# Optimization experiments

Measured on AMD Instinct MI355X. Metric: run time of the kernel, lower is better.

Reference implementation:

```python
import jax, jax.numpy as jnp
import numpy as np

EPS = 1e-5

def layer_norm(x, g, b):
    m = jnp.mean(x, axis=-1, keepdims=True)
    v = jnp.var(x, axis=-1, keepdims=True)
    return (x - m) / jnp.sqrt(v + EPS) * g + b

def mab(Q, K, adj, Wq, Wk, Wv, Wo, g1, b1, g2, b2, H):
    # Q: [B, nq, dq], K: [B, nk, dk], adj: [nk, nk] graph-conv aggregation
    B, nq, _ = Q.shape
    dv = Wq.shape[1]
    dh = dv // H
    Qp = Q @ Wq                                   # [B, nq, dv]
    Kg = jnp.einsum('ij,bjd->bid', adj, K)        # GCN neighborhood aggregation
    Kp = Kg @ Wk                                  # [B, nk, dv]
    Vp = Kg @ Wv                                  # [B, nk, dv]
    Qh = Qp.reshape(B, nq, H, dh)
    Kh = Kp.reshape(B, -1, H, dh)
    Vh = Vp.reshape(B, -1, H, dh)
    scale = 1.0 / np.sqrt(dv).astype(np.float32)
    att = jax.nn.softmax(jnp.einsum('bqhd,bkhd->bhqk', Qh, Kh) * scale, axis=-1)
    Oh = Qh + jnp.einsum('bhqk,bkhd->bqhd', att, Vh)   # residual inside heads
    O = Oh.reshape(B, nq, dv)
    O = layer_norm(O, g1, b1)
    O = O + jax.nn.relu(O @ Wo)
    O = layer_norm(O, g2, b2)
    return O

def setup_inputs() -> dict:
    key = jax.random.key(0)
    ks = jax.random.split(key, 16)
    B, P, D = 16384, 25, 256
    w = lambda k, shp: jax.random.normal(k, shp, dtype=jnp.float32) * 0.05
    adj2 = jax.random.uniform(ks[15], (3, 3), dtype=jnp.float32)
    adj2 = adj2 / jnp.sum(adj2, axis=-1, keepdims=True)  # row-normalized GCN adj
    return {
        'X': jax.random.normal(ks[0], (B, 1, D), dtype=jnp.float32),
        'S1': w(ks[1], (3, 1)),
        'S2': w(ks[2], (P, 3)),
        'adj1': jnp.ones((1, 1), dtype=jnp.float32),
        'adj2': adj2,
        'Wq1': w(ks[3], (D, D)), 'Wk1': w(ks[4], (D, D)),
        'Wv1': w(ks[5], (D, D)), 'Wo1': w(ks[6], (D, D)),
        'g11': jnp.ones((D,), jnp.float32), 'b11': jnp.zeros((D,), jnp.float32),
        'g12': jnp.ones((D,), jnp.float32), 'b12': jnp.zeros((D,), jnp.float32),
        'Wq2': w(ks[7], (D, D)), 'Wk2': w(ks[8], (D, D)),
        'Wv2': w(ks[9], (D, D)), 'Wo2': w(ks[10], (D, D)),
        'g21': jnp.ones((D,), jnp.float32), 'b21': jnp.zeros((D,), jnp.float32),
        'g22': jnp.ones((D,), jnp.float32), 'b22': jnp.zeros((D,), jnp.float32),
        'H': 4,
    }

def reference(X, S1, S2, adj1, adj2,
              Wq1, Wk1, Wv1, Wo1, g11, b11, g12, b12,
              Wq2, Wk2, Wv2, Wo2, g21, b21, g22, b22, H):
    Q1 = jnp.einsum('ij,bjd->bid', S1, X)            # [B, 3, D]
    scale_liner = mab(Q1, X, adj1, Wq1, Wk1, Wv1, Wo1, g11, b11, g12, b12, H)
    Q2 = jnp.einsum('pj,bjd->bpd', S2, scale_liner)  # [B, 25, D]
    scale_graph = mab(Q2, scale_liner, adj2, Wq2, Wk2, Wv2, Wo2, g21, b21, g22, b22, H)
    return scale_graph
```

## Files before the change

kernel.cpp:

```cpp
#include <hip/hip_runtime.h>


typedef __attribute__((ext_vector_type(8))) short bf16x8;
typedef __attribute__((ext_vector_type(4))) float f32x4;

constexpr int D   = 256;
constexpr int AST = 264;
constexpr int KST = 528;

__device__ __forceinline__ short f2bf(float f) {
  unsigned u = __builtin_bit_cast(unsigned, f);
  u = (u + 0x7FFFu + ((u >> 16) & 1u)) >> 16;
  return (short)u;
}
__device__ __forceinline__ float bf2f(short s) {
  unsigned u = ((unsigned)(unsigned short)s) << 16;
  return __builtin_bit_cast(float, u);
}

__global__ void pack_weights(const float* __restrict__ Wq1, const float* __restrict__ Wv1,
                             const float* __restrict__ Wo1, const float* __restrict__ Wq2,
                             const float* __restrict__ Wk2, const float* __restrict__ Wv2,
                             const float* __restrict__ Wo2, short* __restrict__ ws) {
  int g = blockIdx.x * 256 + threadIdx.x;
  int mat = g >> 13, r = g & 8191;
  const float* W = (mat == 0) ? Wq1 : (mat == 1) ? Wv1 : (mat == 2) ? Wo1 :
                   (mat == 3) ? Wq2 : (mat == 4) ? Wk2 : (mat == 5) ? Wv2 : Wo2;
  int nt = r >> 9, s = (r >> 6) & 7, lane = r & 63;
  int qd = lane >> 4, mc = lane & 15;
  bf16x8 v;
#pragma unroll
  for (int j = 0; j < 8; ++j) {
    int k = s * 32 + qd * 8 + j;
    v[j] = f2bf(W[k * 256 + nt * 16 + mc]);
  }
  *reinterpret_cast<bf16x8*>(ws + (size_t)g * 8) = v;
}

template <int MT, int NTW, bool PMODE, bool SYNCMID>
__device__ __forceinline__ void wave_gemm(const short* __restrict__ ub,
                                          const bf16x8* __restrict__ Bp, int nt0,
                                          int lane, short* __restrict__ dst,
                                          int dstStride, int lim) {
  const int m = lane & 15, q = lane >> 4;
  f32x4 acc[MT][NTW];
#pragma unroll
  for (int mt = 0; mt < MT; ++mt)
#pragma unroll
    for (int n = 0; n < NTW; ++n) acc[mt][n] = (f32x4){0.f, 0.f, 0.f, 0.f};

#pragma unroll
  for (int s = 0; s < 8; ++s) {
    bf16x8 a[MT];
#pragma unroll
    for (int mt = 0; mt < MT; ++mt)
      a[mt] = *reinterpret_cast<const bf16x8*>(ub + (mt * 16 + m) * AST + s * 32 + q * 8);
#pragma unroll
    for (int n = 0; n < NTW; ++n) {
      bf16x8 b = Bp[(nt0 + n) * 512 + s * 64 + lane];
#pragma unroll
      for (int mt = 0; mt < MT; ++mt)
        acc[mt][n] = __builtin_amdgcn_mfma_f32_16x16x32_bf16(a[mt], b, acc[mt][n], 0, 0, 0);
    }
  }
  if (SYNCMID) __syncthreads();
#pragma unroll
  for (int mt = 0; mt < MT; ++mt)
#pragma unroll
    for (int n = 0; n < NTW; ++n)
#pragma unroll
      for (int r = 0; r < 4; ++r) {
        int rr = mt * 16 + q * 4 + r;
        bool ok = PMODE ? ((rr & 31) < 25) : (rr < lim);
        if (ok) dst[rr * dstStride + (nt0 + n) * 16 + m] = f2bf(acc[mt][n][r]);
      }
}

__device__ __forceinline__ void ln6(float (&v)[2][3], const float* __restrict__ g,
                                    const float* __restrict__ b, int tid, float* red) {
  const int lane = tid & 63, wv = tid >> 6;
#pragma unroll
  for (int i = 0; i < 6; ++i) {
    float x = v[i / 3][i % 3];
    float s = x, qq = x * x;
#pragma unroll
    for (int mm = 32; mm; mm >>= 1) {
      s += __shfl_xor(s, mm, 64);
      qq += __shfl_xor(qq, mm, 64);
    }
    if (lane == 0) {
      red[(i * 4 + wv) * 2 + 0] = s;
      red[(i * 4 + wv) * 2 + 1] = qq;
    }
  }
  __syncthreads();
  const float gg = g[tid], bb = b[tid];
#pragma unroll
  for (int i = 0; i < 6; ++i) {
    float s = red[(i * 4 + 0) * 2] + red[(i * 4 + 1) * 2] +
              red[(i * 4 + 2) * 2] + red[(i * 4 + 3) * 2];
    float qq = red[(i * 4 + 0) * 2 + 1] + red[(i * 4 + 1) * 2 + 1] +
               red[(i * 4 + 2) * 2 + 1] + red[(i * 4 + 3) * 2 + 1];
    float mean = s * (1.0f / 256.0f);
    float var  = qq * (1.0f / 256.0f) - mean * mean;
    float inv  = rsqrtf(var + 1e-5f);
    float x = v[i / 3][i % 3];
    v[i / 3][i % 3] = (x - mean) * inv * gg + bb;
  }
  __syncthreads();
}

__device__ __forceinline__ void coop_stats(const short* __restrict__ ub, int tid,
                                           float* red, float (*st)[2]) {
  const int rr = tid >> 2, part = tid & 3;
  float s = 0.f, ss = 0.f;
  if ((rr & 31) < 25) {
#pragma unroll
    for (int c = 0; c < 8; ++c) {
      bf16x8 v8 = *reinterpret_cast<const bf16x8*>(ub + rr * AST + part * 64 + c * 8);
#pragma unroll
      for (int j = 0; j < 8; ++j) {
        float f = bf2f(v8[j]);
        s += f;
        ss = fmaf(f, f, ss);
      }
    }
  }
  red[(rr * 4 + part) * 2 + 0] = s;
  red[(rr * 4 + part) * 2 + 1] = ss;
  __syncthreads();
  if (tid < 64) {
    float S = 0.f, SS = 0.f;
#pragma unroll
    for (int i = 0; i < 4; ++i) {
      S  += red[(tid * 4 + i) * 2 + 0];
      SS += red[(tid * 4 + i) * 2 + 1];
    }
    float mean = S * (1.0f / 256.0f);
    float var  = SS * (1.0f / 256.0f) - mean * mean;
    st[tid][0] = mean;
    st[tid][1] = rsqrtf(var + 1e-5f);
  }
}

__global__ __launch_bounds__(256, 2)
void gt_mfma(const float* __restrict__ X, const float* __restrict__ S1,
             const float* __restrict__ S2, const float* __restrict__ adj1,
             const float* __restrict__ adj2,
             const float* __restrict__ g11, const float* __restrict__ b11,
             const float* __restrict__ g12, const float* __restrict__ b12,
             const float* __restrict__ g21, const float* __restrict__ b21,
             const float* __restrict__ g22, const float* __restrict__ b22,
             const short* __restrict__ wsp, float* __restrict__ out) {
  __shared__ __align__(16) short ubuf[64 * AST];
  __shared__ __align__(16) short kvbuf[6 * KST];
  __shared__ __align__(16) short qvbuf[2 * KST];
  __shared__ __align__(16) float wbuf[4][64][4];
  __shared__ float stbuf[64][2];
  __shared__ float redbuf[512];

  const int tid = threadIdx.x, lane = tid & 63, wv = tid >> 6;
  const int b0 = blockIdx.x * 2;

  const bf16x8* pQV1 = (const bf16x8*)(wsp + 0 * 65536);
  const bf16x8* pWo1 = (const bf16x8*)(wsp + 2 * 65536);
  const bf16x8* pWq2 = (const bf16x8*)(wsp + 3 * 65536);
  const bf16x8* pKV2 = (const bf16x8*)(wsp + 4 * 65536);
  const bf16x8* pWo2 = (const bf16x8*)(wsp + 6 * 65536);

  float x0 = X[(size_t)(b0 + 0) * D + tid];
  float x1 = X[(size_t)(b0 + 1) * D + tid];
  ubuf[0 * AST + tid] = f2bf(x0);
  ubuf[1 * AST + tid] = f2bf(x1);
#pragma unroll
  for (int rz = 2; rz < 16; ++rz) ubuf[rz * AST + tid] = 0;
#pragma unroll
  for (int rz = 25; rz < 32; ++rz) ubuf[rz * AST + tid] = 0;
#pragma unroll
  for (int rz = 57; rz < 64; ++rz) ubuf[rz * AST + tid] = 0;
  __syncthreads();

  wave_gemm<1, 8, false, false>(ubuf, pQV1, wv * 8, lane, qvbuf, KST, 2);
  __syncthreads();

  const float a1 = adj1[0];
  float o1[2][3];
#pragma unroll
  for (int b = 0; b < 2; ++b) {
    float xq = bf2f(qvbuf[b * KST + tid]);
    float xv = bf2f(qvbuf[b * KST + 256 + tid]) * a1;
#pragma unroll
    for (int qq = 0; qq < 3; ++qq) o1[b][qq] = fmaf(S1[qq], xq, xv);
  }
  ln6(o1, g11, b11, tid, redbuf);

#pragma unroll
  for (int b = 0; b < 2; ++b)
#pragma unroll
    for (int qq = 0; qq < 3; ++qq) ubuf[(b * 3 + qq) * AST + tid] = f2bf(o1[b][qq]);
  __syncthreads();
  wave_gemm<1, 4, false, false>(ubuf, pWo1, wv * 4, lane, kvbuf, KST, 6);
  __syncthreads();
#pragma unroll
  for (int b = 0; b < 2; ++b)
#pragma unroll
    for (int qq = 0; qq < 3; ++qq)
      o1[b][qq] += fmaxf(bf2f(kvbuf[(b * 3 + qq) * KST + tid]), 0.f);
  ln6(o1, g12, b12, tid, redbuf);

#pragma unroll
  for (int b = 0; b < 2; ++b)
#pragma unroll
    for (int i = 0; i < 3; ++i) {
      float kg = adj2[i * 3 + 0] * o1[b][0] + adj2[i * 3 + 1] * o1[b][1] +
                 adj2[i * 3 + 2] * o1[b][2];
      ubuf[(b * 3 + i) * AST + tid] = f2bf(kg);
    }
  __syncthreads();
  wave_gemm<1, 8, false, false>(ubuf, pKV2, wv * 8, lane, kvbuf, KST, 6);
  __syncthreads();

#pragma unroll
  for (int b = 0; b < 2; ++b)
#pragma unroll
    for (int p = 0; p < 25; ++p) {
      float q2 = S2[p * 3 + 0] * o1[b][0] + S2[p * 3 + 1] * o1[b][1] +
                 S2[p * 3 + 2] * o1[b][2];
      ubuf[(b * 32 + p) * AST + tid] = f2bf(q2);
    }
  __syncthreads();
  wave_gemm<4, 4, true, true>(ubuf, pWq2, wv * 4, lane, ubuf, AST, 0);
  __syncthreads();

  {
    const int mt = wv, bb = wv >> 1, plb = (wv & 1) * 16;
    const int m = lane & 15, q = lane >> 4;
#pragma unroll
    for (int h = 0; h < 4; ++h) {
      f32x4 sa = (f32x4){0.f, 0.f, 0.f, 0.f};
#pragma unroll
      for (int s = 0; s < 2; ++s) {
        bf16x8 aq = *reinterpret_cast<const bf16x8*>(
            ubuf + (mt * 16 + m) * AST + h * 64 + s * 32 + q * 8);
        bf16x8 bk = (bf16x8){0, 0, 0, 0, 0, 0, 0, 0};
        if (m < 3)
          bk = *reinterpret_cast<const bf16x8*>(
              kvbuf + (bb * 3 + m) * KST + h * 64 + s * 32 + q * 8);
        sa = __builtin_amdgcn_mfma_f32_16x16x32_bf16(aq, bk, sa, 0, 0, 0);
      }
#pragma unroll
      for (int r = 0; r < 4; ++r) {
        float sc = sa[r] * 0.0625f;
        int lb = lane & 48;
        float t0 = __shfl(sc, lb + 0), t1 = __shfl(sc, lb + 1), t2 = __shfl(sc, lb + 2);
        float mx = fmaxf(t0, fmaxf(t1, t2));
        float e0 = __expf(t0 - mx), e1 = __expf(t1 - mx), e2 = __expf(t2 - mx);
        float w = __expf(sc - mx) / (e0 + e1 + e2);
        int pl = plb + q * 4 + r;
        if (m < 3 && pl < 25) wbuf[h][bb * 32 + pl][m] = w;
      }
    }
  }
  __syncthreads();

  float acc[2][25];
#pragma unroll
  for (int b = 0; b < 2; ++b) {
    float vp0 = bf2f(kvbuf[(b * 3 + 0) * KST + 256 + tid]);
    float vp1 = bf2f(kvbuf[(b * 3 + 1) * KST + 256 + tid]);
    float vp2 = bf2f(kvbuf[(b * 3 + 2) * KST + 256 + tid]);
#pragma unroll
    for (int p = 0; p < 25; ++p) {
      float4 w4 = *reinterpret_cast<const float4*>(&wbuf[wv][b * 32 + p][0]);
      float qpv = bf2f(ubuf[(b * 32 + p) * AST + tid]);
      float x = qpv + w4.x * vp0 + w4.y * vp1 + w4.z * vp2;
      acc[b][p] = x;
      ubuf[(b * 32 + p) * AST + tid] = f2bf(x);
    }
  }
  __syncthreads();

  coop_stats(ubuf, tid, redbuf, stbuf);
  __syncthreads();
  {
    const float gg = g21[tid], bb2 = b21[tid];
#pragma unroll
    for (int b = 0; b < 2; ++b)
#pragma unroll
      for (int p = 0; p < 25; ++p) {
        int rr = b * 32 + p;
        acc[b][p] = (acc[b][p] - stbuf[rr][0]) * stbuf[rr][1] * gg + bb2;
      }
  }

#pragma unroll
  for (int b = 0; b < 2; ++b)
#pragma unroll
    for (int p = 0; p < 25; ++p) ubuf[(b * 32 + p) * AST + tid] = f2bf(acc[b][p]);
  __syncthreads();
  wave_gemm<4, 4, true, true>(ubuf, pWo2, wv * 4, lane, ubuf, AST, 0);
  __syncthreads();

#pragma unroll
  for (int b = 0; b < 2; ++b)
#pragma unroll
    for (int p = 0; p < 25; ++p) {
      float r = bf2f(ubuf[(b * 32 + p) * AST + tid]);
      float x = acc[b][p] + fmaxf(r, 0.f);
      acc[b][p] = x;
      ubuf[(b * 32 + p) * AST + tid] = f2bf(x);
    }
  __syncthreads();
  coop_stats(ubuf, tid, redbuf, stbuf);
  __syncthreads();
  {
    const float gg = g22[tid], bb2 = b22[tid];
#pragma unroll
    for (int b = 0; b < 2; ++b)
#pragma unroll
      for (int p = 0; p < 25; ++p) {
        int rr = b * 32 + p;
        float v = (acc[b][p] - stbuf[rr][0]) * stbuf[rr][1] * gg + bb2;
        out[((size_t)(b0 + b) * 25 + p) * D + tid] = v;
      }
  }
}

extern "C" void kernel_launch(void* const* d_in, const int* in_sizes, int n_in,
                              void* d_out, int out_size, void* d_ws, size_t ws_size,
                              hipStream_t stream) {
  const float* X    = (const float*)d_in[0];
  const float* S1   = (const float*)d_in[1];
  const float* S2   = (const float*)d_in[2];
  const float* adj1 = (const float*)d_in[3];
  const float* adj2 = (const float*)d_in[4];
  const float* Wq1  = (const float*)d_in[5];
  const float* Wv1  = (const float*)d_in[7];
  const float* Wo1  = (const float*)d_in[8];
  const float* g11  = (const float*)d_in[9];
  const float* b11  = (const float*)d_in[10];
  const float* g12  = (const float*)d_in[11];
  const float* b12  = (const float*)d_in[12];
  const float* Wq2  = (const float*)d_in[13];
  const float* Wk2  = (const float*)d_in[14];
  const float* Wv2  = (const float*)d_in[15];
  const float* Wo2  = (const float*)d_in[16];
  const float* g21  = (const float*)d_in[17];
  const float* b21  = (const float*)d_in[18];
  const float* g22  = (const float*)d_in[19];
  const float* b22  = (const float*)d_in[20];

  short* wsp = (short*)d_ws;

  hipLaunchKernelGGL(pack_weights, dim3(224), dim3(256), 0, stream,
                     Wq1, Wv1, Wo1, Wq2, Wk2, Wv2, Wo2, wsp);

  const int B = in_sizes[0] / D;
  hipLaunchKernelGGL(gt_mfma, dim3(B / 2), dim3(256), 0, stream,
                     X, S1, S2, adj1, adj2, g11, b11, g12, b12,
                     g21, b21, g22, b22, (const short*)wsp, (float*)d_out);
}
```

Measured before the change: 1.133 ms.

## Factor S2 through Wq2 so stage-2 query projection runs on 3 rows

Uses linearity: Q2 = S2·scale_liner, so Q2·Wq2 = S2·(scale_liner·Wq2). The kernel now projects only the 6 scale_liner rows through Wq2 together with the K/V projections in one fused 12-tile GEMM, then expands the scores and queries with S2 in registers. This replaces the 64-row Wq2 GEMM and shrinks shared memory. Launch bounds go to 3 blocks per SM and the Wo2 GEMM is split into two halves to reduce register pressure. Rounding now happens in a different order relative to the bf16 casts, and the tighter register budget may cause spills.

```diff
diff --git a/kernel.cpp b/kernel.cpp
--- a/kernel.cpp
+++ b/kernel.cpp
@@ -6,7 +6,7 @@
 
 constexpr int D   = 256;
 constexpr int AST = 264;
-constexpr int KST = 528;
+constexpr int SST = 264;
 
 __device__ __forceinline__ short f2bf(float f) {
   unsigned u = __builtin_bit_cast(unsigned, f);
@@ -76,6 +76,37 @@
       }
 }
 
+__device__ __forceinline__ void gemm_qkv(const short* __restrict__ ub,
+                                         const bf16x8* __restrict__ Bp, int nt0,
+                                         int lane, short* __restrict__ sb) {
+  const int m = lane & 15, q = lane >> 4;
+  f32x4 acc[12];
+#pragma unroll
+  for (int n = 0; n < 12; ++n) acc[n] = (f32x4){0.f, 0.f, 0.f, 0.f};
+#pragma unroll
+  for (int s = 0; s < 8; ++s) {
+    bf16x8 a = *reinterpret_cast<const bf16x8*>(ub + m * AST + s * 32 + q * 8);
+#pragma unroll
+    for (int n = 0; n < 12; ++n) {
+      bf16x8 b = Bp[(nt0 + n) * 512 + s * 64 + lane];
+      acc[n] = __builtin_amdgcn_mfma_f32_16x16x32_bf16(a, b, acc[n], 0, 0, 0);
+    }
+  }
+#pragma unroll
+  for (int n = 0; n < 12; ++n) {
+    int nt = nt0 + n;
+    int mat = nt >> 4;
+    int lo = (mat == 0) ? 0 : 6;
+    int col = (nt & 15) * 16 + m;
+#pragma unroll
+    for (int r = 0; r < 4; ++r) {
+      int rr = q * 4 + r;
+      if (rr >= lo && rr < lo + 6)
+        sb[(mat * 6 + rr - lo) * SST + col] = f2bf(acc[n][r]);
+    }
+  }
+}
+
 __device__ __forceinline__ void ln6(float (&v)[2][3], const float* __restrict__ g,
                                     const float* __restrict__ b, int tid, float* red) {
   const int lane = tid & 63, wv = tid >> 6;
@@ -143,7 +174,7 @@
   }
 }
 
-__global__ __launch_bounds__(256, 2)
+__global__ __launch_bounds__(256, 3)
 void gt_mfma(const float* __restrict__ X, const float* __restrict__ S1,
              const float* __restrict__ S2, const float* __restrict__ adj1,
              const float* __restrict__ adj2,
@@ -153,9 +184,9 @@
              const float* __restrict__ g22, const float* __restrict__ b22,
              const short* __restrict__ wsp, float* __restrict__ out) {
   __shared__ __align__(16) short ubuf[64 * AST];
-  __shared__ __align__(16) short kvbuf[6 * KST];
-  __shared__ __align__(16) short qvbuf[2 * KST];
+  __shared__ __align__(16) short sbuf[18 * SST];
   __shared__ __align__(16) float wbuf[4][64][4];
+  __shared__ float slkbuf[4][6][3];
   __shared__ float stbuf[64][2];
   __shared__ float redbuf[512];
 
@@ -164,31 +195,26 @@
 
   const bf16x8* pQV1 = (const bf16x8*)(wsp + 0 * 65536);
   const bf16x8* pWo1 = (const bf16x8*)(wsp + 2 * 65536);
-  const bf16x8* pWq2 = (const bf16x8*)(wsp + 3 * 65536);
-  const bf16x8* pKV2 = (const bf16x8*)(wsp + 4 * 65536);
+  const bf16x8* pQKV = (const bf16x8*)(wsp + 3 * 65536);
   const bf16x8* pWo2 = (const bf16x8*)(wsp + 6 * 65536);
+
+  short* qv = sbuf + 6 * SST;
 
   float x0 = X[(size_t)(b0 + 0) * D + tid];
   float x1 = X[(size_t)(b0 + 1) * D + tid];
   ubuf[0 * AST + tid] = f2bf(x0);
   ubuf[1 * AST + tid] = f2bf(x1);
-#pragma unroll
-  for (int rz = 2; rz < 16; ++rz) ubuf[rz * AST + tid] = 0;
-#pragma unroll
-  for (int rz = 25; rz < 32; ++rz) ubuf[rz * AST + tid] = 0;
-#pragma unroll
-  for (int rz = 57; rz < 64; ++rz) ubuf[rz * AST + tid] = 0;
-  __syncthreads();
-
-  wave_gemm<1, 8, false, false>(ubuf, pQV1, wv * 8, lane, qvbuf, KST, 2);
+  __syncthreads();
+
+  wave_gemm<1, 8, false, false>(ubuf, pQV1, wv * 8, lane, qv, 528, 2);
   __syncthreads();
 
   const float a1 = adj1[0];
   float o1[2][3];
 #pragma unroll
   for (int b = 0; b < 2; ++b) {
-    float xq = bf2f(qvbuf[b * KST + tid]);
-    float xv = bf2f(qvbuf[b * KST + 256 + tid]) * a1;
+    float xq = bf2f(qv[b * 528 + tid]);
+    float xv = bf2f(qv[b * 528 + 256 + tid]) * a1;
 #pragma unroll
     for (int qq = 0; qq < 3; ++qq) o1[b][qq] = fmaf(S1[qq], xq, xv);
   }
@@ -199,82 +225,87 @@
 #pragma unroll
     for (int qq = 0; qq < 3; ++qq) ubuf[(b * 3 + qq) * AST + tid] = f2bf(o1[b][qq]);
   __syncthreads();
-  wave_gemm<1, 4, false, false>(ubuf, pWo1, wv * 4, lane, kvbuf, KST, 6);
+  wave_gemm<1, 4, false, false>(ubuf, pWo1, wv * 4, lane, sbuf, SST, 6);
   __syncthreads();
 #pragma unroll
   for (int b = 0; b < 2; ++b)
 #pragma unroll
     for (int qq = 0; qq < 3; ++qq)
-      o1[b][qq] += fmaxf(bf2f(kvbuf[(b * 3 + qq) * KST + tid]), 0.f);
+      o1[b][qq] += fmaxf(bf2f(sbuf[(b * 3 + qq) * SST + tid]), 0.f);
   ln6(o1, g12, b12, tid, redbuf);
 
+#pragma unroll
+  for (int b = 0; b < 2; ++b)
+#pragma unroll
+    for (int qq = 0; qq < 3; ++qq) ubuf[(b * 3 + qq) * AST + tid] = f2bf(o1[b][qq]);
 #pragma unroll
   for (int b = 0; b < 2; ++b)
 #pragma unroll
     for (int i = 0; i < 3; ++i) {
       float kg = adj2[i * 3 + 0] * o1[b][0] + adj2[i * 3 + 1] * o1[b][1] +
                  adj2[i * 3 + 2] * o1[b][2];
-      ubuf[(b * 3 + i) * AST + tid] = f2bf(kg);
-    }
-  __syncthreads();
-  wave_gemm<1, 8, false, false>(ubuf, pKV2, wv * 8, lane, kvbuf, KST, 6);
-  __syncthreads();
-
-#pragma unroll
-  for (int b = 0; b < 2; ++b)
-#pragma unroll
-    for (int p = 0; p < 25; ++p) {
-      float q2 = S2[p * 3 + 0] * o1[b][0] + S2[p * 3 + 1] * o1[b][1] +
-                 S2[p * 3 + 2] * o1[b][2];
-      ubuf[(b * 32 + p) * AST + tid] = f2bf(q2);
-    }
-  __syncthreads();
-  wave_gemm<4, 4, true, true>(ubuf, pWq2, wv * 4, lane, ubuf, AST, 0);
+      ubuf[(6 + b * 3 + i) * AST + tid] = f2bf(kg);
+    }
+  __syncthreads();
+
+  gemm_qkv(ubuf, pQKV, wv * 12, lane, sbuf);
   __syncthreads();
 
   {
-    const int mt = wv, bb = wv >> 1, plb = (wv & 1) * 16;
     const int m = lane & 15, q = lane >> 4;
-#pragma unroll
-    for (int h = 0; h < 4; ++h) {
-      f32x4 sa = (f32x4){0.f, 0.f, 0.f, 0.f};
-#pragma unroll
-      for (int s = 0; s < 2; ++s) {
-        bf16x8 aq = *reinterpret_cast<const bf16x8*>(
-            ubuf + (mt * 16 + m) * AST + h * 64 + s * 32 + q * 8);
-        bf16x8 bk = (bf16x8){0, 0, 0, 0, 0, 0, 0, 0};
-        if (m < 3)
-          bk = *reinterpret_cast<const bf16x8*>(
-              kvbuf + (bb * 3 + m) * KST + h * 64 + s * 32 + q * 8);
-        sa = __builtin_amdgcn_mfma_f32_16x16x32_bf16(aq, bk, sa, 0, 0, 0);
-      }
-#pragma unroll
-      for (int r = 0; r < 4; ++r) {
-        float sc = sa[r] * 0.0625f;
-        int lb = lane & 48;
-        float t0 = __shfl(sc, lb + 0), t1 = __shfl(sc, lb + 1), t2 = __shfl(sc, lb + 2);
-        float mx = fmaxf(t0, fmaxf(t1, t2));
-        float e0 = __expf(t0 - mx), e1 = __expf(t1 - mx), e2 = __expf(t2 - mx);
-        float w = __expf(sc - mx) / (e0 + e1 + e2);
-        int pl = plb + q * 4 + r;
-        if (m < 3 && pl < 25) wbuf[h][bb * 32 + pl][m] = w;
-      }
-    }
-  }
-  __syncthreads();
-
-  float acc[2][25];
+    f32x4 sa = (f32x4){0.f, 0.f, 0.f, 0.f};
+#pragma unroll
+    for (int s = 0; s < 2; ++s) {
+      bf16x8 aq = *reinterpret_cast<const bf16x8*>(
+          sbuf + m * SST + wv * 64 + s * 32 + q * 8);
+      bf16x8 bk = (bf16x8){0, 0, 0, 0, 0, 0, 0, 0};
+      if (m < 6)
+        bk = *reinterpret_cast<const bf16x8*>(
+            sbuf + (6 + m) * SST + wv * 64 + s * 32 + q * 8);
+      sa = __builtin_amdgcn_mfma_f32_16x16x32_bf16(aq, bk, sa, 0, 0, 0);
+    }
+#pragma unroll
+    for (int r = 0; r < 4; ++r) {
+      int i = q * 4 + r;
+      if (i < 6 && m < 6 && ((i >= 3) == (m >= 3)))
+        slkbuf[wv][i][m % 3] = sa[r] * 0.0625f;
+    }
+    int b = lane >> 5, p = lane & 31;
+    if (p < 25) {
+      float sc0 = 0.f, sc1 = 0.f, sc2 = 0.f;
+#pragma unroll
+      for (int ii = 0; ii < 3; ++ii) {
+        float s2v = S2[p * 3 + ii];
+        sc0 = fmaf(s2v, slkbuf[wv][b * 3 + ii][0], sc0);
+        sc1 = fmaf(s2v, slkbuf[wv][b * 3 + ii][1], sc1);
+        sc2 = fmaf(s2v, slkbuf[wv][b * 3 + ii][2], sc2);
+      }
+      float mx = fmaxf(sc0, fmaxf(sc1, sc2));
+      float e0 = __expf(sc0 - mx), e1 = __expf(sc1 - mx), e2 = __expf(sc2 - mx);
+      float inv = 1.f / (e0 + e1 + e2);
+      wbuf[wv][b * 32 + p][0] = e0 * inv;
+      wbuf[wv][b * 32 + p][1] = e1 * inv;
+      wbuf[wv][b * 32 + p][2] = e2 * inv;
+      wbuf[wv][b * 32 + p][3] = 0.f;
+    }
+  }
+  __syncthreads();
+
+  float accv[2][25];
 #pragma unroll
   for (int b = 0; b < 2; ++b) {
-    float vp0 = bf2f(kvbuf[(b * 3 + 0) * KST + 256 + tid]);
-    float vp1 = bf2f(kvbuf[(b * 3 + 1) * KST + 256 + tid]);
-    float vp2 = bf2f(kvbuf[(b * 3 + 2) * KST + 256 + tid]);
+    float slq0 = bf2f(sbuf[(b * 3 + 0) * SST + tid]);
+    float slq1 = bf2f(sbuf[(b * 3 + 1) * SST + tid]);
+    float slq2 = bf2f(sbuf[(b * 3 + 2) * SST + tid]);
+    float vp0 = bf2f(sbuf[(12 + b * 3 + 0) * SST + tid]);
+    float vp1 = bf2f(sbuf[(12 + b * 3 + 1) * SST + tid]);
+    float vp2 = bf2f(sbuf[(12 + b * 3 + 2) * SST + tid]);
 #pragma unroll
     for (int p = 0; p < 25; ++p) {
       float4 w4 = *reinterpret_cast<const float4*>(&wbuf[wv][b * 32 + p][0]);
-      float qpv = bf2f(ubuf[(b * 32 + p) * AST + tid]);
+      float qpv = S2[p * 3 + 0] * slq0 + S2[p * 3 + 1] * slq1 + S2[p * 3 + 2] * slq2;
       float x = qpv + w4.x * vp0 + w4.y * vp1 + w4.z * vp2;
-      acc[b][p] = x;
+      accv[b][p] = x;
       ubuf[(b * 32 + p) * AST + tid] = f2bf(x);
     }
   }
@@ -289,16 +320,17 @@
 #pragma unroll
       for (int p = 0; p < 25; ++p) {
         int rr = b * 32 + p;
-        acc[b][p] = (acc[b][p] - stbuf[rr][0]) * stbuf[rr][1] * gg + bb2;
-      }
-  }
-
-#pragma unroll
-  for (int b = 0; b < 2; ++b)
-#pragma unroll
-    for (int p = 0; p < 25; ++p) ubuf[(b * 32 + p) * AST + tid] = f2bf(acc[b][p]);
-  __syncthreads();
-  wave_gemm<4, 4, true, true>(ubuf, pWo2, wv * 4, lane, ubuf, AST, 0);
+        accv[b][p] = (accv[b][p] - stbuf[rr][0]) * stbuf[rr][1] * gg + bb2;
+      }
+  }
+
+#pragma unroll
+  for (int b = 0; b < 2; ++b)
+#pragma unroll
+    for (int p = 0; p < 25; ++p) ubuf[(b * 32 + p) * AST + tid] = f2bf(accv[b][p]);
+  __syncthreads();
+  wave_gemm<2, 4, true, true>(ubuf, pWo2, wv * 4, lane, ubuf, AST, 0);
+  wave_gemm<2, 4, true, true>(ubuf + 32 * AST, pWo2, wv * 4, lane, ubuf + 32 * AST, AST, 0);
   __syncthreads();
 
 #pragma unroll
@@ -306,8 +338,8 @@
 #pragma unroll
     for (int p = 0; p < 25; ++p) {
       float r = bf2f(ubuf[(b * 32 + p) * AST + tid]);
-      float x = acc[b][p] + fmaxf(r, 0.f);
-      acc[b][p] = x;
+      float x = accv[b][p] + fmaxf(r, 0.f);
+      accv[b][p] = x;
       ubuf[(b * 32 + p) * AST + tid] = f2bf(x);
     }
   __syncthreads();
@@ -320,7 +352,7 @@
 #pragma unroll
       for (int p = 0; p < 25; ++p) {
         int rr = b * 32 + p;
-        float v = (acc[b][p] - stbuf[rr][0]) * stbuf[rr][1] * gg + bb2;
+        float v = (accv[b][p] - stbuf[rr][0]) * stbuf[rr][1] * gg + bb2;
         out[((size_t)(b0 + b) * 25 + p) * D + tid] = v;
       }
   }
```

New measurement: 972.6 us. -14.2%, faster.
